# Performance work log

Measured on AMD Instinct MI355X. Metric: run time of the kernel, lower is better.

## Reference

```python
import jax, jax.numpy as jnp
import numpy as np

H = 8  # num_heads (init kwarg)

def setup_inputs() -> dict:
    key = jax.random.key(0)
    k1, k2, k3, k4 = jax.random.split(key, 4)
    B, S, E = 4, 2048, 512
    x = jax.random.normal(k1, (B, S, E), dtype=jnp.float32)
    # 'normal' keras initializer ~ N(0, 0.05)
    Wq = jax.random.normal(k2, (E, E), dtype=jnp.float32) * 0.05
    Wk = jax.random.normal(k3, (E, E), dtype=jnp.float32) * 0.05
    Wv = jax.random.normal(k4, (E, E), dtype=jnp.float32) * 0.05
    return {"x": x, "Wq": Wq, "Wk": Wk, "Wv": Wv}

def _split_heads(t):
    # [B,S,E] -> [H,B,S,E/H]; matches tf.stack(tf.split(t, H, axis=2))
    B, S, E = t.shape
    return t.reshape(B, S, H, E // H).transpose(2, 0, 1, 3)

def reference(x, Wq, Wk, Wv):
    B, S, E = x.shape
    q = _split_heads(jnp.einsum('bse,ef->bsf', x, Wq))  # [H,B,S,dh]
    k = _split_heads(jnp.einsum('bse,ef->bsf', x, Wk))
    v = _split_heads(jnp.einsum('bse,ef->bsf', x, Wv))
    # NOTE: original has NO 1/sqrt(d) scaling
    scores = jnp.einsum('hbqd,hbkd->hbqk', q, k)         # [H,B,S,S]
    attn = jax.nn.softmax(scores, axis=-1)
    effect = jnp.einsum('hbqk,hbkd->hbqd', attn, v)      # [H,B,S,dh]
    # tf.concat(tf.split(effect, H), axis=-1) + squeeze == merge heads on last dim
    out = effect.transpose(1, 2, 0, 3).reshape(B, S, E)  # [B,S,E]
    return (out, x)
```

## Files before the change

kernel.cpp:

```cpp
#include <hip/hip_runtime.h>

typedef _Float16 f16x8 __attribute__((ext_vector_type(8)));
typedef __fp16 h16x2 __attribute__((ext_vector_type(2)));
typedef float f32x4 __attribute__((ext_vector_type(4)));
typedef float f32x16 __attribute__((ext_vector_type(16)));

#define GF(r) ((((r)&3)) ^ (((r)>>2)&3))
#define LOG2E 1.44269504088896f

#define GLD16(gp, lp) __builtin_amdgcn_global_load_lds( \
    (const __attribute__((address_space(1))) void*)(gp), \
    (__attribute__((address_space(3))) void*)(lp), 16, 0, 0)

__global__ void cvt_all_kernel(const float4* __restrict__ x4, f16x8* __restrict__ xh,
                               float4* __restrict__ xc,
                               const float* __restrict__ Wq, const float* __restrict__ Wk,
                               const float* __restrict__ Wv, _Float16* __restrict__ wt) {
    const int blk = blockIdx.x;
    if (blk < 2048) {
        int i = blk * 256 + threadIdx.x;
        float4 a = x4[2 * i], b = x4[2 * i + 1];
        xc[2 * i] = a;
        xc[2 * i + 1] = b;
        f16x8 h;
        h[0] = (_Float16)a.x; h[1] = (_Float16)a.y; h[2] = (_Float16)a.z; h[3] = (_Float16)a.w;
        h[4] = (_Float16)b.x; h[5] = (_Float16)b.y; h[6] = (_Float16)b.z; h[7] = (_Float16)b.w;
        xh[i] = h;
    } else {
        int j = (blk - 2048) * 256 + threadIdx.x;
        int mat = j >> 18;
        int r = (j >> 9) & 511;
        int n = j & 511;
        const float* W = (mat == 0) ? Wq : ((mat == 1) ? Wk : Wv);
        float v = W[r * 512 + n];
        wt[(size_t)mat * 262144 + (size_t)n * 512 + r] = (_Float16)v;
    }
}

__global__ __launch_bounds__(256, 2) void gemm_qkv(
    const _Float16* __restrict__ xh, const _Float16* __restrict__ wt,
    _Float16* __restrict__ qh, _Float16* __restrict__ kh, _Float16* __restrict__ vt) {
    __shared__ __align__(16) char gsm[49152];
    const int mat = blockIdx.y;
    const _Float16* wp = wt + (size_t)mat * 262144;
    const int mtile = blockIdx.x >> 2, ntile = blockIdx.x & 3;
    const int tid = threadIdx.x, lane = tid & 63;
    const int g = lane >> 4, c = lane & 15;
    const int wid = tid >> 6, wm = wid >> 1, wn = wid & 1;

    f32x4 acc[4][4];
#pragma unroll
    for (int i = 0; i < 4; ++i)
#pragma unroll
        for (int j = 0; j < 4; ++j) acc[i][j] = (f32x4){0.f, 0.f, 0.f, 0.f};

    const int row0 = tid >> 2, p0 = tid & 3;

    auto GSTAGE = [&](int buf, int ks) {
        _Float16* la_ = (_Float16*)(gsm + buf * 16384);
        _Float16* lb_ = (_Float16*)(gsm + buf * 16384 + 8192);
        int r = row0, pp = p0 ^ GF(r);
        GLD16(xh + (size_t)(mtile * 128 + r) * 512 + ks * 32 + pp * 8, &la_[tid * 8]);
        GLD16(wp + (size_t)(ntile * 128 + r) * 512 + ks * 32 + pp * 8, &lb_[tid * 8]);
        r = 64 + row0; pp = p0 ^ GF(r);
        GLD16(xh + (size_t)(mtile * 128 + r) * 512 + ks * 32 + pp * 8, &la_[(256 + tid) * 8]);
        GLD16(wp + (size_t)(ntile * 128 + r) * 512 + ks * 32 + pp * 8, &lb_[(256 + tid) * 8]);
    };

    auto GTILE = [&](int ks) {
        const _Float16* la = (const _Float16*)(gsm + (ks % 3) * 16384);
        const _Float16* lb = (const _Float16*)(gsm + (ks % 3) * 16384 + 8192);
        f16x8 af[4], bf[4];
#pragma unroll
        for (int i = 0; i < 4; ++i) {
            int ra = wm * 64 + i * 16 + c;
            af[i] = *(const f16x8*)&la[ra * 32 + ((g ^ GF(ra)) * 8)];
            int rb = wn * 64 + i * 16 + c;
            bf[i] = *(const f16x8*)&lb[rb * 32 + ((g ^ GF(rb)) * 8)];
        }
        __builtin_amdgcn_s_setprio(1);
#pragma unroll
        for (int mi = 0; mi < 4; ++mi)
#pragma unroll
            for (int ni = 0; ni < 4; ++ni)
                acc[mi][ni] = __builtin_amdgcn_mfma_f32_16x16x32_f16(af[mi], bf[ni], acc[mi][ni], 0, 0, 0);
        __builtin_amdgcn_s_setprio(0);
    };

    GSTAGE(0, 0); GSTAGE(1, 1);
#pragma unroll 1
    for (int ks = 0; ks < 14; ++ks) {
        asm volatile("s_waitcnt vmcnt(4)" ::: "memory");
        __builtin_amdgcn_s_barrier();
        __builtin_amdgcn_sched_barrier(0);
        GSTAGE((ks + 2) % 3, ks + 2);
        GTILE(ks);
    }
    asm volatile("s_waitcnt vmcnt(4)" ::: "memory");
    __builtin_amdgcn_s_barrier();
    GTILE(14);
    asm volatile("s_waitcnt vmcnt(0)" ::: "memory");
    __builtin_amdgcn_s_barrier();
    GTILE(15);

#pragma unroll
    for (int mi = 0; mi < 4; ++mi)
#pragma unroll
        for (int ni = 0; ni < 4; ++ni)
#pragma unroll
            for (int r = 0; r < 4; ++r) {
                int m = mtile * 128 + wm * 64 + mi * 16 + g * 4 + r;
                int n = ntile * 128 + wn * 64 + ni * 16 + c;
                _Float16 hv = (_Float16)acc[mi][ni][r];
                if (mat == 0) {
                    qh[(size_t)m * 512 + n] = hv;
                } else if (mat == 1) {
                    kh[(size_t)m * 512 + n] = hv;
                } else {
                    int h = n >> 6, d = n & 63, bb = m >> 11, s = m & 2047;
                    vt[(((size_t)h * 4 + bb) * 64 + d) * 2048 + s] = hv;
                }
            }
}

__global__ __launch_bounds__(512, 4) void attn_kernel(
    const _Float16* __restrict__ qh, const _Float16* __restrict__ kh,
    const _Float16* __restrict__ vt, float* __restrict__ out) {
    __shared__ __align__(16) char smem[36864];

    const int bid = blockIdx.x;
    const int xcd = bid & 7, idx = bid >> 3;
    const int hb = xcd * 4 + (idx >> 4);
    const int qblk = idx & 15;
    const int h = hb >> 2, b = hb & 3;
    const int tid = threadIdx.x, lane = tid & 63, wid = tid >> 6;
    const int qg = wid & 3, half = wid >> 2;
    const int q = lane & 31, hi = lane >> 5;

    const int qrow0 = qblk * 128 + qg * 32;
    const _Float16* qp = qh + ((size_t)b * 2048 + qrow0) * 512 + h * 64;
    const _Float16* kp = kh + (size_t)b * 2048 * 512 + h * 64;
    const _Float16* vp = vt + (size_t)hb * 64 * 2048;

    const int sHalf = tid >> 8, stt = tid & 255;
    const int krow = stt >> 3;
    const int kch = (stt & 7) ^ ((krow ^ (krow >> 3)) & 7);
    const int vrow = stt >> 2;
    const int vch = (stt & 3) ^ ((vrow ^ (vrow >> 2)) & 3);

    auto STAGE = [&](int i) {
        char* base = smem + (i & 1) * 16384;
        const int kvt = sHalf * 32 + i;
        GLD16(kp + ((size_t)(kvt * 32 + krow) * 512) + kch * 8, (_Float16*)base + tid * 8);
        GLD16(vp + (size_t)vrow * 2048 + kvt * 32 + vch * 8, (_Float16*)(base + 8192) + tid * 8);
    };

    f16x8 aQ[4];
#pragma unroll
    for (int kc = 0; kc < 4; ++kc)
        aQ[kc] = *(const f16x8*)(qp + (size_t)q * 512 + kc * 16 + hi * 8);

    float mrow = -1e30f, lrow = 0.f;
    f32x16 o0, o1;
#pragma unroll
    for (int i = 0; i < 16; ++i) { o0[i] = 0.f; o1[i] = 0.f; }

    const h16x2 ONE2 = {(__fp16)1.0f, (__fp16)1.0f};
    const int swk = (q ^ (q >> 3)) & 7;
    const int swv0 = (q ^ (q >> 2)) & 3;
    const int swv1 = ((32 + q) ^ ((32 + q) >> 2)) & 3;

    auto TILE = [&](int it) {
        const _Float16* kb = (const _Float16*)(smem + (it & 1) * 16384 + half * 4096);
        const _Float16* vb = (const _Float16*)(smem + (it & 1) * 16384 + 8192 + half * 4096);

        f32x16 s0;
        __builtin_amdgcn_s_setprio(1);
        {
            f32x16 z;
#pragma unroll
            for (int i = 0; i < 16; ++i) z[i] = 0.f;
#pragma unroll
            for (int kc = 0; kc < 4; ++kc) {
                f16x8 ak = *(const f16x8*)&kb[q * 64 + (((2 * kc + hi) ^ swk) * 8)];
                z = __builtin_amdgcn_mfma_f32_32x32x16_f16(ak, aQ[kc], z, 0, 0, 0);
            }
            s0 = z;
        }
        __builtin_amdgcn_s_setprio(0);

        float pm;
        {
            float m0 = fmaxf(fmaxf(fmaxf(s0[0], s0[1]), s0[2]), s0[3]);
            float m1 = fmaxf(fmaxf(fmaxf(s0[4], s0[5]), s0[6]), s0[7]);
            float m2 = fmaxf(fmaxf(fmaxf(s0[8], s0[9]), s0[10]), s0[11]);
            float m3 = fmaxf(fmaxf(fmaxf(s0[12], s0[13]), s0[14]), s0[15]);
            pm = fmaxf(fmaxf(m0, m1), fmaxf(m2, m3));
        }
        pm = fmaxf(pm, __shfl_xor(pm, 32));
        if (__any(pm > mrow + 8.0f)) {
            const float nm = fmaxf(mrow, pm);
            const float e = __builtin_amdgcn_exp2f((mrow - nm) * LOG2E);
            mrow = nm;
            lrow *= e;
            o0 *= e;
            o1 *= e;
        }
        const float nm2 = mrow * LOG2E;

#pragma unroll
        for (int i = 0; i < 16; ++i)
            s0[i] = __builtin_amdgcn_exp2f(fmaf(s0[i], LOG2E, -nm2));

        f16x8 pf[2];
        float rs = 0.f;
        {
            h16x2 p0 = __builtin_amdgcn_cvt_pkrtz(s0[0], s0[1]);
            h16x2 p1 = __builtin_amdgcn_cvt_pkrtz(s0[2], s0[3]);
            h16x2 p2 = __builtin_amdgcn_cvt_pkrtz(s0[4], s0[5]);
            h16x2 p3 = __builtin_amdgcn_cvt_pkrtz(s0[6], s0[7]);
            h16x2 p4 = __builtin_amdgcn_cvt_pkrtz(s0[8], s0[9]);
            h16x2 p5 = __builtin_amdgcn_cvt_pkrtz(s0[10], s0[11]);
            h16x2 p6 = __builtin_amdgcn_cvt_pkrtz(s0[12], s0[13]);
            h16x2 p7 = __builtin_amdgcn_cvt_pkrtz(s0[14], s0[15]);
            rs = __builtin_amdgcn_fdot2(p0, ONE2, rs, false);
            rs = __builtin_amdgcn_fdot2(p1, ONE2, rs, false);
            rs = __builtin_amdgcn_fdot2(p2, ONE2, rs, false);
            rs = __builtin_amdgcn_fdot2(p3, ONE2, rs, false);
            rs = __builtin_amdgcn_fdot2(p4, ONE2, rs, false);
            rs = __builtin_amdgcn_fdot2(p5, ONE2, rs, false);
            rs = __builtin_amdgcn_fdot2(p6, ONE2, rs, false);
            rs = __builtin_amdgcn_fdot2(p7, ONE2, rs, false);
            unsigned t0 = __builtin_bit_cast(unsigned, p0);
            unsigned t1 = __builtin_bit_cast(unsigned, p1);
            unsigned t2 = __builtin_bit_cast(unsigned, p2);
            unsigned t3 = __builtin_bit_cast(unsigned, p3);
            unsigned t4 = __builtin_bit_cast(unsigned, p4);
            unsigned t5 = __builtin_bit_cast(unsigned, p5);
            unsigned t6 = __builtin_bit_cast(unsigned, p6);
            unsigned t7 = __builtin_bit_cast(unsigned, p7);
            asm volatile("v_permlane32_swap_b32 %0, %1" : "+v"(t0), "+v"(t2));
            asm volatile("v_permlane32_swap_b32 %0, %1" : "+v"(t1), "+v"(t3));
            asm volatile("v_permlane32_swap_b32 %0, %1" : "+v"(t4), "+v"(t6));
            asm volatile("v_permlane32_swap_b32 %0, %1" : "+v"(t5), "+v"(t7));
            uint4 u0; u0.x = t0; u0.y = t1; u0.z = t2; u0.w = t3;
            uint4 u1; u1.x = t4; u1.y = t5; u1.z = t6; u1.w = t7;
            pf[0] = __builtin_bit_cast(f16x8, u0);
            pf[1] = __builtin_bit_cast(f16x8, u1);
        }
        lrow += rs;

        __builtin_amdgcn_s_setprio(1);
        {
#pragma unroll
            for (int ck = 0; ck < 2; ++ck) {
                f16x8 av0 = *(const f16x8*)&vb[q * 32 + (((2 * ck + hi) ^ swv0) * 8)];
                f16x8 av1 = *(const f16x8*)&vb[(32 + q) * 32 + (((2 * ck + hi) ^ swv1) * 8)];
                o0 = __builtin_amdgcn_mfma_f32_32x32x16_f16(av0, pf[ck], o0, 0, 0, 0);
                o1 = __builtin_amdgcn_mfma_f32_32x32x16_f16(av1, pf[ck], o1, 0, 0, 0);
            }
        }
        __builtin_amdgcn_s_setprio(0);
    };

    STAGE(0);
#pragma unroll 1
    for (int it = 0; it < 32; ++it) {
        asm volatile("s_waitcnt vmcnt(0)" ::: "memory");
        __builtin_amdgcn_s_barrier();
        __builtin_amdgcn_sched_barrier(0);
        if (it < 31) STAGE(it + 1);
        TILE(it);
    }

    lrow += __shfl_xor(lrow, 32);
    __builtin_amdgcn_s_barrier();

    float* xg = (float*)smem + qg * 2112;
    if (half) {
#pragma unroll
        for (int i = 0; i < 16; ++i) {
            xg[i * 64 + lane] = o0[i];
            xg[(16 + i) * 64 + lane] = o1[i];
        }
        if (!hi) { xg[2048 + q] = mrow; xg[2080 + q] = lrow; }
    }
    __syncthreads();
    if (!half) {
        const float m_b = xg[2048 + q], l_b = xg[2080 + q];
        const float m = fmaxf(mrow, m_b);
        const float e_a = __builtin_amdgcn_exp2f((mrow - m) * LOG2E);
        const float e_b = __builtin_amdgcn_exp2f((m_b - m) * LOG2E);
        const float inv = 1.0f / (lrow * e_a + l_b * e_b);
        const float sa = e_a * inv, sb = e_b * inv;
#pragma unroll
        for (int i = 0; i < 16; ++i) {
            o0[i] = o0[i] * sa + xg[i * 64 + lane] * sb;
            o1[i] = o1[i] * sa + xg[(16 + i) * 64 + lane] * sb;
        }
        asm volatile("s_waitcnt lgkmcnt(0)" ::: "memory");
#pragma unroll
        for (int i = 0; i < 16; ++i) {
            int dr = (i & 3) + 8 * (i >> 2) + 4 * hi;
            xg[dr * 33 + q] = o0[i];
            xg[(32 + dr) * 33 + q] = o1[i];
        }
        __builtin_amdgcn_s_waitcnt(0);
        const int d0c = (lane & 15) * 4;
#pragma unroll
        for (int i2 = 0; i2 < 8; ++i2) {
            int qr = 4 * i2 + (lane >> 4);
            float4 v;
            v.x = xg[(d0c + 0) * 33 + qr];
            v.y = xg[(d0c + 1) * 33 + qr];
            v.z = xg[(d0c + 2) * 33 + qr];
            v.w = xg[(d0c + 3) * 33 + qr];
            *(float4*)(out + ((size_t)b * 2048 + qrow0 + qr) * 512 + h * 64 + d0c) = v;
        }
    }
}

extern "C" void kernel_launch(void* const* d_in, const int* in_sizes, int n_in,
                              void* d_out, int out_size, void* d_ws, size_t ws_size,
                              hipStream_t stream) {
    const float* x = (const float*)d_in[0];
    const float* Wq = (const float*)d_in[1];
    const float* Wk = (const float*)d_in[2];
    const float* Wv = (const float*)d_in[3];
    float* out = (float*)d_out;
    float* xcopy = out + 4194304;

    char* ws = (char*)d_ws;
    _Float16* xh = (_Float16*)ws;
    _Float16* wt = (_Float16*)(ws + (size_t)(10u << 20));
    _Float16* qh = (_Float16*)(ws + (size_t)(12u << 20));
    _Float16* kh = (_Float16*)(ws + (size_t)(20u << 20));
    _Float16* vt = (_Float16*)(ws + (size_t)(28u << 20));

    cvt_all_kernel<<<5120, 256, 0, stream>>>((const float4*)x, (f16x8*)xh, (float4*)xcopy,
                                             Wq, Wk, Wv, wt);
    gemm_qkv<<<dim3(256, 3), 256, 0, stream>>>(xh, wt, qh, kh, vt);
    attn_kernel<<<512, 512, 0, stream>>>(qh, kh, vt, out);
}
```

Measured before the change: 93.63 us.

## Software-pipeline QK^T of next KV tile with softmax/PV using 4-slot LDS ring

Replaces the double-buffered KV staging with a 4-slot LDS ring (64 KB) that keeps two tiles in flight, waiting with vmcnt(2) instead of draining all loads. The loop is unrolled by two so the QK^T MFMAs for tile t run before the softmax and PV of tile t-1, letting matrix work overlap the exp/convert VALU work. The row-sum fdot2 chain is also split into two accumulators to shorten the dependency chain. The larger LDS footprint cuts how many 512-thread blocks fit per CU below what launch_bounds(512,4) asks for. The vmcnt(2) wait near the final tiles may not cover the last stage, which risks a race.

```diff
diff --git a/kernel.cpp b/kernel.cpp
--- a/kernel.cpp
+++ b/kernel.cpp
@@ -126,7 +126,7 @@
 __global__ __launch_bounds__(512, 4) void attn_kernel(
     const _Float16* __restrict__ qh, const _Float16* __restrict__ kh,
     const _Float16* __restrict__ vt, float* __restrict__ out) {
-    __shared__ __align__(16) char smem[36864];
+    __shared__ __align__(16) char smem[65536];
 
     const int bid = blockIdx.x;
     const int xcd = bid & 7, idx = bid >> 3;
@@ -149,10 +149,10 @@
     const int vch = (stt & 3) ^ ((vrow ^ (vrow >> 2)) & 3);
 
     auto STAGE = [&](int i) {
-        char* base = smem + (i & 1) * 16384;
+        char* base = smem + (i & 3) * 16384 + sHalf * 8192;
         const int kvt = sHalf * 32 + i;
-        GLD16(kp + ((size_t)(kvt * 32 + krow) * 512) + kch * 8, (_Float16*)base + tid * 8);
-        GLD16(vp + (size_t)vrow * 2048 + kvt * 32 + vch * 8, (_Float16*)(base + 8192) + tid * 8);
+        GLD16(kp + ((size_t)(kvt * 32 + krow) * 512) + kch * 8, (_Float16*)base + stt * 8);
+        GLD16(vp + (size_t)vrow * 2048 + kvt * 32 + vch * 8, (_Float16*)(base + 4096) + stt * 8);
     };
 
     f16x8 aQ[4];
@@ -170,25 +170,28 @@
     const int swv0 = (q ^ (q >> 2)) & 3;
     const int swv1 = ((32 + q) ^ ((32 + q) >> 2)) & 3;
 
-    auto TILE = [&](int it) {
-        const _Float16* kb = (const _Float16*)(smem + (it & 1) * 16384 + half * 4096);
-        const _Float16* vb = (const _Float16*)(smem + (it & 1) * 16384 + 8192 + half * 4096);
-
-        f32x16 s0;
+    auto KPTR = [&](int t) {
+        return (const _Float16*)(smem + (t & 3) * 16384 + half * 8192);
+    };
+    auto VPTR = [&](int t) {
+        return (const _Float16*)(smem + (t & 3) * 16384 + half * 8192 + 4096);
+    };
+
+    auto QKT = [&](const _Float16* kb, f32x16& s) {
+        f32x16 z;
+#pragma unroll
+        for (int i = 0; i < 16; ++i) z[i] = 0.f;
         __builtin_amdgcn_s_setprio(1);
-        {
-            f32x16 z;
-#pragma unroll
-            for (int i = 0; i < 16; ++i) z[i] = 0.f;
-#pragma unroll
-            for (int kc = 0; kc < 4; ++kc) {
-                f16x8 ak = *(const f16x8*)&kb[q * 64 + (((2 * kc + hi) ^ swk) * 8)];
-                z = __builtin_amdgcn_mfma_f32_32x32x16_f16(ak, aQ[kc], z, 0, 0, 0);
-            }
-            s0 = z;
+#pragma unroll
+        for (int kc = 0; kc < 4; ++kc) {
+            f16x8 ak = *(const f16x8*)&kb[q * 64 + (((2 * kc + hi) ^ swk) * 8)];
+            z = __builtin_amdgcn_mfma_f32_32x32x16_f16(ak, aQ[kc], z, 0, 0, 0);
         }
         __builtin_amdgcn_s_setprio(0);
-
+        s = z;
+    };
+
+    auto SMPV = [&](f32x16& s0, const _Float16* vb) {
         float pm;
         {
             float m0 = fmaxf(fmaxf(fmaxf(s0[0], s0[1]), s0[2]), s0[3]);
@@ -207,13 +210,12 @@
             o1 *= e;
         }
         const float nm2 = mrow * LOG2E;
-
 #pragma unroll
         for (int i = 0; i < 16; ++i)
             s0[i] = __builtin_amdgcn_exp2f(fmaf(s0[i], LOG2E, -nm2));
 
         f16x8 pf[2];
-        float rs = 0.f;
+        float rsA = 0.f, rsB = 0.f;
         {
             h16x2 p0 = __builtin_amdgcn_cvt_pkrtz(s0[0], s0[1]);
             h16x2 p1 = __builtin_amdgcn_cvt_pkrtz(s0[2], s0[3]);
@@ -223,14 +225,14 @@
             h16x2 p5 = __builtin_amdgcn_cvt_pkrtz(s0[10], s0[11]);
             h16x2 p6 = __builtin_amdgcn_cvt_pkrtz(s0[12], s0[13]);
             h16x2 p7 = __builtin_amdgcn_cvt_pkrtz(s0[14], s0[15]);
-            rs = __builtin_amdgcn_fdot2(p0, ONE2, rs, false);
-            rs = __builtin_amdgcn_fdot2(p1, ONE2, rs, false);
-            rs = __builtin_amdgcn_fdot2(p2, ONE2, rs, false);
-            rs = __builtin_amdgcn_fdot2(p3, ONE2, rs, false);
-            rs = __builtin_amdgcn_fdot2(p4, ONE2, rs, false);
-            rs = __builtin_amdgcn_fdot2(p5, ONE2, rs, false);
-            rs = __builtin_amdgcn_fdot2(p6, ONE2, rs, false);
-            rs = __builtin_amdgcn_fdot2(p7, ONE2, rs, false);
+            rsA = __builtin_amdgcn_fdot2(p0, ONE2, rsA, false);
+            rsB = __builtin_amdgcn_fdot2(p1, ONE2, rsB, false);
+            rsA = __builtin_amdgcn_fdot2(p2, ONE2, rsA, false);
+            rsB = __builtin_amdgcn_fdot2(p3, ONE2, rsB, false);
+            rsA = __builtin_amdgcn_fdot2(p4, ONE2, rsA, false);
+            rsB = __builtin_amdgcn_fdot2(p5, ONE2, rsB, false);
+            rsA = __builtin_amdgcn_fdot2(p6, ONE2, rsA, false);
+            rsB = __builtin_amdgcn_fdot2(p7, ONE2, rsB, false);
             unsigned t0 = __builtin_bit_cast(unsigned, p0);
             unsigned t1 = __builtin_bit_cast(unsigned, p1);
             unsigned t2 = __builtin_bit_cast(unsigned, p2);
@@ -248,29 +250,41 @@
             pf[0] = __builtin_bit_cast(f16x8, u0);
             pf[1] = __builtin_bit_cast(f16x8, u1);
         }
-        lrow += rs;
+        lrow += rsA + rsB;
 
         __builtin_amdgcn_s_setprio(1);
-        {
-#pragma unroll
-            for (int ck = 0; ck < 2; ++ck) {
-                f16x8 av0 = *(const f16x8*)&vb[q * 32 + (((2 * ck + hi) ^ swv0) * 8)];
-                f16x8 av1 = *(const f16x8*)&vb[(32 + q) * 32 + (((2 * ck + hi) ^ swv1) * 8)];
-                o0 = __builtin_amdgcn_mfma_f32_32x32x16_f16(av0, pf[ck], o0, 0, 0, 0);
-                o1 = __builtin_amdgcn_mfma_f32_32x32x16_f16(av1, pf[ck], o1, 0, 0, 0);
-            }
+#pragma unroll
+        for (int ck = 0; ck < 2; ++ck) {
+            f16x8 av0 = *(const f16x8*)&vb[q * 32 + (((2 * ck + hi) ^ swv0) * 8)];
+            f16x8 av1 = *(const f16x8*)&vb[(32 + q) * 32 + (((2 * ck + hi) ^ swv1) * 8)];
+            o0 = __builtin_amdgcn_mfma_f32_32x32x16_f16(av0, pf[ck], o0, 0, 0, 0);
+            o1 = __builtin_amdgcn_mfma_f32_32x32x16_f16(av1, pf[ck], o1, 0, 0, 0);
         }
         __builtin_amdgcn_s_setprio(0);
     };
 
-    STAGE(0);
+#define WAITBAR() do { \
+    asm volatile("s_waitcnt vmcnt(2)" ::: "memory"); \
+    __builtin_amdgcn_s_barrier(); \
+    __builtin_amdgcn_sched_barrier(0); \
+} while (0)
+
+    f32x16 sA, sB;
+    STAGE(0); STAGE(1);
+    WAITBAR();
+    STAGE(2);
+    QKT(KPTR(0), sA);
+
 #pragma unroll 1
-    for (int it = 0; it < 32; ++it) {
-        asm volatile("s_waitcnt vmcnt(0)" ::: "memory");
-        __builtin_amdgcn_s_barrier();
-        __builtin_amdgcn_sched_barrier(0);
-        if (it < 31) STAGE(it + 1);
-        TILE(it);
+    for (int t = 1; t < 32; t += 2) {
+        WAITBAR();
+        if (t + 2 < 32) STAGE(t + 2);
+        QKT(KPTR(t), sB);
+        SMPV(sA, VPTR(t - 1));
+        WAITBAR();
+        if (t + 3 < 32) STAGE(t + 3);
+        if (t + 1 < 32) QKT(KPTR(t + 1), sA);
+        SMPV(sB, VPTR(t));
     }
 
     lrow += __shfl_xor(lrow, 32);
@@ -318,6 +332,7 @@
             *(float4*)(out + ((size_t)b * 2048 + qrow0 + qr) * 512 + h * 64 + d0c) = v;
         }
     }
+#undef WAITBAR
 }
 
 extern "C" void kernel_launch(void* const* d_in, const int* in_sizes, int n_in,
```

After: 94.68 us. Within noise of the previous version (+1.1%).
